# Optimization experiments

Measured on AMD Instinct MI355X. Metric: run time of the kernel, lower is better.

The kernel has to match this reference:

```python
import jax, jax.numpy as jnp
import numpy as np

F = 256      # n_features
N = 128      # n_nodes
B = 4096     # batch


def setup_inputs() -> dict:
    key = jax.random.key(0)
    ks = jax.random.split(key, 11)
    s = lambda *sh: 1.0 / np.sqrt(sh[-2]) if len(sh) >= 2 else 1.0
    x = jax.random.normal(ks[0], (B, F), dtype=jnp.float32)
    # Block-diagonal weights: [F, in, out] per stage; biases [F, out]
    w1 = jax.random.normal(ks[1], (F, 1, N), dtype=jnp.float32)
    b1 = jax.random.normal(ks[2], (F, N), dtype=jnp.float32) * 0.01
    w2 = jax.random.normal(ks[3], (F, N, N), dtype=jnp.float32) / np.sqrt(N)
    b2 = jax.random.normal(ks[4], (F, N), dtype=jnp.float32) * 0.01
    w3 = jax.random.normal(ks[5], (F, N, N), dtype=jnp.float32) / np.sqrt(N)
    b3 = jax.random.normal(ks[6], (F, N), dtype=jnp.float32) * 0.01
    w4 = jax.random.normal(ks[7], (F, N, 1), dtype=jnp.float32) / np.sqrt(N)
    b4 = jax.random.normal(ks[8], (F, 1), dtype=jnp.float32) * 0.01
    # Final linear: [F, 1] weight, [1] bias
    lr_w = jax.random.normal(ks[9], (F, 1), dtype=jnp.float32) / np.sqrt(F)
    lr_b = jax.random.normal(ks[10], (1,), dtype=jnp.float32) * 0.01
    return {"x": x, "w1": w1, "b1": b1, "w2": w2, "b2": b2,
            "w3": w3, "b3": b3, "w4": w4, "b4": b4,
            "lr_w": lr_w, "lr_b": lr_b}


def reference(x, w1, b1, w2, b2, w3, b3, w4, b4, lr_w, lr_b):
    # Per-feature block-diagonal MLP chain with ReLU between stages.
    # x: [B, F] -> view each feature as a 1-dim input to its own subnet.
    h = x[:, :, None]                                   # [B, F, 1]
    h = jax.nn.relu(jnp.einsum('bfi,fio->bfo', h, w1) + b1)   # [B, F, N]
    h = jax.nn.relu(jnp.einsum('bfi,fio->bfo', h, w2) + b2)   # [B, F, N]
    h = jax.nn.relu(jnp.einsum('bfi,fio->bfo', h, w3) + b3)   # [B, F, N]
    h = jnp.einsum('bfi,fio->bfo', h, w4) + b4                # [B, F, 1]
    x_pre = h[:, :, 0]                                        # [B, F]
    return x_pre @ lr_w + lr_b                                # [B, 1]
```

## Files before the change

### kernel.cpp

```cpp
#include <hip/hip_runtime.h>
#include <hip/hip_bf16.h>

#define F_DIM 256
#define N_DIM 128
#define B_DIM 4096

typedef float f32x2v __attribute__((ext_vector_type(2)));
typedef float f32x4v __attribute__((ext_vector_type(4)));
typedef float f32x16v __attribute__((ext_vector_type(16)));
typedef short s16x8 __attribute__((ext_vector_type(8)));
typedef unsigned int u32x4v __attribute__((ext_vector_type(4)));

#define PIN(x) asm("" : "+v"(x))

__device__ __forceinline__ unsigned short f2bf(float f) {
  union { float f; unsigned u; } v; v.f = f;
  unsigned r = v.u + 0x7fffu + ((v.u >> 16) & 1u);
  return (unsigned short)(r >> 16);
}

__device__ __forceinline__ unsigned pk2(float a, float b) {
  union { __hip_bfloat16 h[2]; unsigned u; } v;
  v.h[0] = __float2bfloat16(a);
  v.h[1] = __float2bfloat16(b);
  return v.u;
}

__device__ __forceinline__ void gload16(const void* g, void* l) {
  __builtin_amdgcn_global_load_lds(
      (const __attribute__((address_space(1))) unsigned int*)g,
      (__attribute__((address_space(3))) unsigned int*)l, 16, 0, 0);
}

__device__ __forceinline__ s16x8 frag1(unsigned d) {
  u32x4v v = {d, 0u, 0u, 0u};
  return __builtin_bit_cast(s16x8, v);
}

struct frag2 { s16x8 lo, hi; };

__device__ __forceinline__ frag2 cvt2(f32x16v a) {
  unsigned P[8];
#pragma unroll
  for (int q = 0; q < 8; ++q) {
    unsigned pk = pk2(a[2 * q], a[2 * q + 1]);
    asm("v_pk_max_i16 %0, %1, 0" : "=v"(P[q]) : "v"(pk));
  }
  u32x4v lo = {P[0], P[1], P[2], P[3]};
  u32x4v hh = {P[4], P[5], P[6], P[7]};
  frag2 r;
  r.lo = __builtin_bit_cast(s16x8, lo);
  r.hi = __builtin_bit_cast(s16x8, hh);
  return r;
}

__global__ void prep_w(const float* __restrict__ w2, const float* __restrict__ w3,
                       unsigned int* __restrict__ wTs) {
  __shared__ float tile[128 * 130];
  int m = blockIdx.x;
  const float* src = (m < 256) ? (w2 + (size_t)m * 16384)
                               : (w3 + (size_t)(m - 256) * 16384);
  int t = threadIdx.x;
  for (int k = 0; k < 64; ++k) {
    int idx = k * 256 + t;
    int i = idx >> 7, o = idx & 127;
    tile[o * 130 + i] = src[idx];
  }
  __syncthreads();
  unsigned int* dst = wTs + (size_t)m * 8192;
  for (int k = 0; k < 32; ++k) {
    int idx = k * 256 + t;
    int o = idx >> 6, i2 = idx & 63;
    unsigned pk = (unsigned)f2bf(tile[o * 130 + 2 * i2]) |
                  ((unsigned)f2bf(tile[o * 130 + 2 * i2 + 1]) << 16);
    int w = i2 & 7;
    int i2p = (i2 & ~7) + ((w >> 1) & 1) * 4 + (w & 1) + (((w >> 2) & 1) << 1);
    dst[(o * 64) + (i2p ^ ((o & 15) << 2))] = pk;
  }
}

__global__ void prep_x(const float* __restrict__ x, float* __restrict__ xT) {
  __shared__ float tile[64][65];
  int btile = blockIdx.x & 63;
  int ftile = blockIdx.x >> 6;
  int t = threadIdx.x;
  for (int k = 0; k < 16; ++k) {
    int idx = k * 256 + t;
    int r = idx >> 6, c = idx & 63;
    tile[r][c] = x[(size_t)(btile * 64 + r) * F_DIM + ftile * 64 + c];
  }
  __syncthreads();
  for (int k = 0; k < 16; ++k) {
    int idx = k * 256 + t;
    int fr = idx >> 6, br = idx & 63;
    xT[(size_t)(ftile * 64 + fr) * B_DIM + btile * 64 + br] = tile[br][fr];
  }
}

__global__ __launch_bounds__(512, 2) void mlp_chain(
    const float* __restrict__ xT, const float* __restrict__ w1,
    const float* __restrict__ b1, const float* __restrict__ b2,
    const float* __restrict__ b3, const float* __restrict__ w4,
    const float* __restrict__ b4, const unsigned int* __restrict__ wTs,
    float* __restrict__ xp) {
  __shared__ __align__(16) char Wb[2][128 * 256];
  __shared__ __align__(16) float w4l[N_DIM];

  const int f    = blockIdx.x >> 1;
  const int half = blockIdx.x & 1;
  const int t    = threadIdx.x;
  const int lane = t & 63, wid = t >> 6;
  const int c32 = lane & 31, hi = lane >> 5;

  {
    const char* s2 = (const char*)(wTs + (size_t)f * 8192);
    const char* s3 = (const char*)(wTs + (size_t)(256 + f) * 8192);
#pragma unroll
    for (int c = 0; c < 4; ++c) {
      int off = (wid * 4 + c) * 1024;
      gload16(s2 + off + lane * 16, &Wb[0][off]);
    }
#pragma unroll
    for (int c = 0; c < 4; ++c) {
      int off = (wid * 4 + c) * 1024;
      gload16(s3 + off + lane * 16, &Wb[1][off]);
    }
    if (t < 32) *(f32x4v*)&w4l[t * 4] = *(const f32x4v*)&w4[f * N_DIM + t * 4];
  }

  unsigned a1d[4], a2d[4], a3d[4];
#pragma unroll
  for (int it = 0; it < 4; ++it) {
    int i = it * 32 + c32;
    float w1v = w1[f * N_DIM + i], b1v = b1[f * N_DIM + i];
    float b2v = b2[f * N_DIM + i], b3v = b3[f * N_DIM + i];
    a1d[it] = hi ? 0u : pk2(w1v, b1v);
    a2d[it] = hi ? 0u : pk2(0.f, b2v);
    a3d[it] = hi ? 0u : pk2(0.f, b3v);
  }
  const float b4f = b4[f];
  const float* xcol = xT + (size_t)f * B_DIM + half * 2048;
  float* xprow = xp + (size_t)f * B_DIM + half * 2048;

  const int wbase = c32 * 256 + (((lane & 15) ^ hi) << 4);
  int va[8];
#pragma unroll
  for (int m = 0; m < 8; ++m) { va[m] = wbase ^ (m << 5); PIN(va[m]); }
  const char* wb = &Wb[0][0];

  __syncthreads();

  const f32x16v zero = {0.f, 0.f, 0.f, 0.f, 0.f, 0.f, 0.f, 0.f,
                        0.f, 0.f, 0.f, 0.f, 0.f, 0.f, 0.f, 0.f};
  const f32x2v zz = {0.f, 0.f};

  float xv = xcol[wid * 32 + c32];
#pragma unroll 1
  for (int itb = 0; itb < 8; ++itb) {
    const int bb = itb * 256 + wid * 32;
    s16x8 Bx = frag1(hi ? 0u : pk2(xv, 1.0f));
    float xv_n = (itb < 7) ? xcol[bb + 256 + c32] : 0.f;

    s16x8 h1[8];
#pragma unroll
    for (int it = 0; it < 4; ++it) {
      f32x16v h = __builtin_amdgcn_mfma_f32_32x32x16_bf16(frag1(a1d[it]), Bx,
                                                          zero, 0, 0, 0);
      frag2 r = cvt2(h);
      h1[2 * it] = r.lo;  h1[2 * it + 1] = r.hi;
      PIN(h1[2 * it]);  PIN(h1[2 * it + 1]);
    }

    s16x8 h2[8];
#pragma unroll
    for (int ntp = 0; ntp < 2; ++ntp) {
      const int nt0 = 2 * ntp, nt1 = nt0 + 1;
      f32x16v u0 = __builtin_amdgcn_mfma_f32_32x32x16_bf16(frag1(a2d[nt0]), Bx,
                                                           zero, 0, 0, 0);
      f32x16v u1 = __builtin_amdgcn_mfma_f32_32x32x16_bf16(frag1(a2d[nt1]), Bx,
                                                           zero, 0, 0, 0);
      __builtin_amdgcn_s_setprio(1);
#pragma unroll
      for (int m = 0; m < 8; ++m) {
        s16x8 af0 = *(const s16x8*)(wb + va[m] + nt0 * 8192);
        s16x8 af1 = *(const s16x8*)(wb + va[m] + nt1 * 8192);
        u0 = __builtin_amdgcn_mfma_f32_32x32x16_bf16(af0, h1[m], u0, 0, 0, 0);
        u1 = __builtin_amdgcn_mfma_f32_32x32x16_bf16(af1, h1[m], u1, 0, 0, 0);
      }
      __builtin_amdgcn_s_setprio(0);
      frag2 r0 = cvt2(u0);
      h2[2 * nt0] = r0.lo;  h2[2 * nt0 + 1] = r0.hi;
      PIN(h2[2 * nt0]);  PIN(h2[2 * nt0 + 1]);
      frag2 r1 = cvt2(u1);
      h2[2 * nt1] = r1.lo;  h2[2 * nt1 + 1] = r1.hi;
      PIN(h2[2 * nt1]);  PIN(h2[2 * nt1 + 1]);
    }

    f32x2v p0 = zz, p1 = zz;
#pragma unroll
    for (int n3p = 0; n3p < 2; ++n3p) {
      const int n30 = 2 * n3p, n31 = n30 + 1;
      f32x16v v0 = __builtin_amdgcn_mfma_f32_32x32x16_bf16(frag1(a3d[n30]), Bx,
                                                           zero, 0, 0, 0);
      f32x16v v1 = __builtin_amdgcn_mfma_f32_32x32x16_bf16(frag1(a3d[n31]), Bx,
                                                           zero, 0, 0, 0);
      __builtin_amdgcn_s_setprio(1);
#pragma unroll
      for (int k = 0; k < 8; ++k) {
        s16x8 af0 = *(const s16x8*)(wb + va[k] + 32768 + n30 * 8192);
        s16x8 af1 = *(const s16x8*)(wb + va[k] + 32768 + n31 * 8192);
        v0 = __builtin_amdgcn_mfma_f32_32x32x16_bf16(af0, h2[k], v0, 0, 0, 0);
        v1 = __builtin_amdgcn_mfma_f32_32x32x16_bf16(af1, h2[k], v1, 0, 0, 0);
      }
      __builtin_amdgcn_s_setprio(0);
#pragma unroll
      for (int q = 0; q < 4; ++q) {
        f32x2v w01_0 = *(const f32x2v*)&w4l[n30 * 32 + q * 8 + hi * 4];
        f32x2v w23_0 = *(const f32x2v*)&w4l[n30 * 32 + q * 8 + hi * 4 + 2];
        f32x2v w01_1 = *(const f32x2v*)&w4l[n31 * 32 + q * 8 + hi * 4];
        f32x2v w23_1 = *(const f32x2v*)&w4l[n31 * 32 + q * 8 + hi * 4 + 2];
        f32x2v r;
        r[0] = fmaxf(v0[4 * q + 0], 0.f); r[1] = fmaxf(v0[4 * q + 1], 0.f);
        p0 += r * w01_0;
        r[0] = fmaxf(v0[4 * q + 2], 0.f); r[1] = fmaxf(v0[4 * q + 3], 0.f);
        p1 += r * w23_0;
        r[0] = fmaxf(v1[4 * q + 0], 0.f); r[1] = fmaxf(v1[4 * q + 1], 0.f);
        p0 += r * w01_1;
        r[0] = fmaxf(v1[4 * q + 2], 0.f); r[1] = fmaxf(v1[4 * q + 3], 0.f);
        p1 += r * w23_1;
      }
    }
    float p = p0[0] + p0[1] + p1[0] + p1[1];
    p += __shfl_xor(p, 32, 64);
    if (hi == 0) xprow[bb + c32] = p + b4f;
    xv = xv_n;
  }
}

__global__ void final_reduce(const float* __restrict__ xp,
                             const float* __restrict__ lr_w,
                             const float* __restrict__ lr_b,
                             float* __restrict__ out) {
  __shared__ float lw[F_DIM];
  __shared__ float part[4][64];
  int t = threadIdx.x;
  if (t < F_DIM) lw[t] = lr_w[t];
  __syncthreads();
  int q = t >> 6, bl = t & 63;
  int b = blockIdx.x * 64 + bl;
  float acc = 0.f;
#pragma unroll 8
  for (int j = 0; j < 64; ++j) {
    int ff = q * 64 + j;
    acc += xp[(size_t)ff * B_DIM + b] * lw[ff];
  }
  part[q][bl] = acc;
  __syncthreads();
  if (q == 0)
    out[b] = part[0][bl] + part[1][bl] + part[2][bl] + part[3][bl] + lr_b[0];
}

extern "C" void kernel_launch(void* const* d_in, const int* in_sizes, int n_in,
                              void* d_out, int out_size, void* d_ws, size_t ws_size,
                              hipStream_t stream) {
  (void)in_sizes; (void)n_in; (void)out_size; (void)ws_size;
  const float* x    = (const float*)d_in[0];
  const float* w1   = (const float*)d_in[1];
  const float* b1   = (const float*)d_in[2];
  const float* w2   = (const float*)d_in[3];
  const float* b2   = (const float*)d_in[4];
  const float* w3   = (const float*)d_in[5];
  const float* b3   = (const float*)d_in[6];
  const float* w4   = (const float*)d_in[7];
  const float* b4   = (const float*)d_in[8];
  const float* lr_w = (const float*)d_in[9];
  const float* lr_b = (const float*)d_in[10];
  float* out = (float*)d_out;

  char* ws = (char*)d_ws;
  unsigned int* wTs = (unsigned int*)ws;
  float* xT = (float*)(ws + (16u << 20));
  float* xp = (float*)(ws + (16u << 20) + (4u << 20));

  prep_w<<<512, 256, 0, stream>>>(w2, w3, wTs);
  prep_x<<<256, 256, 0, stream>>>(x, xT);
  mlp_chain<<<512, 512, 0, stream>>>(xT, w1, b1, b2, b3, w4, b4, wTs, xp);
  final_reduce<<<64, 256, 0, stream>>>(xp, lr_w, lr_b, out);
}
```

Baseline: 99.25 us.

## Keep per-feature W2/W3 fragments in registers and split output columns across waves

Restructures the MLP kernel so that each of 4 waves owns one 32-column output tile of W2 and W3 and holds those weight fragments in registers, instead of staging the full weights in LDS and reading them on every batch tile. The layer-2 output is exchanged through a small LDS buffer with a block barrier, and the layer-4 partial sums are reduced across waves through shared memory. The grid grows to 8 blocks per feature, each covering 512 batch rows. This removes repeated LDS weight reads, but adds two __syncthreads per batch tile, reloads W2/W3 from global memory in every block, and drops the prefetch of x.

```diff
diff --git a/kernel.cpp b/kernel.cpp
--- a/kernel.cpp
+++ b/kernel.cpp
@@ -24,12 +24,6 @@
   v.h[0] = __float2bfloat16(a);
   v.h[1] = __float2bfloat16(b);
   return v.u;
-}
-
-__device__ __forceinline__ void gload16(const void* g, void* l) {
-  __builtin_amdgcn_global_load_lds(
-      (const __attribute__((address_space(1))) unsigned int*)g,
-      (__attribute__((address_space(3))) unsigned int*)l, 16, 0, 0);
 }
 
 __device__ __forceinline__ s16x8 frag1(unsigned d) {
@@ -97,56 +91,47 @@
   }
 }
 
-__global__ __launch_bounds__(512, 2) void mlp_chain(
+__global__ __launch_bounds__(256, 3) void mlp_wreg(
     const float* __restrict__ xT, const float* __restrict__ w1,
     const float* __restrict__ b1, const float* __restrict__ b2,
     const float* __restrict__ b3, const float* __restrict__ w4,
     const float* __restrict__ b4, const unsigned int* __restrict__ wTs,
     float* __restrict__ xp) {
-  __shared__ __align__(16) char Wb[2][128 * 256];
+  __shared__ __align__(16) char xch[8192];
   __shared__ __align__(16) float w4l[N_DIM];
-
-  const int f    = blockIdx.x >> 1;
-  const int half = blockIdx.x & 1;
-  const int t    = threadIdx.x;
+  __shared__ float part[4][32];
+
+  const int f  = blockIdx.x >> 3;
+  const int oc = blockIdx.x & 7;
+  const int t  = threadIdx.x;
   const int lane = t & 63, wid = t >> 6;
   const int c32 = lane & 31, hi = lane >> 5;
 
-  {
-    const char* s2 = (const char*)(wTs + (size_t)f * 8192);
-    const char* s3 = (const char*)(wTs + (size_t)(256 + f) * 8192);
-#pragma unroll
-    for (int c = 0; c < 4; ++c) {
-      int off = (wid * 4 + c) * 1024;
-      gload16(s2 + off + lane * 16, &Wb[0][off]);
-    }
-#pragma unroll
-    for (int c = 0; c < 4; ++c) {
-      int off = (wid * 4 + c) * 1024;
-      gload16(s3 + off + lane * 16, &Wb[1][off]);
-    }
-    if (t < 32) *(f32x4v*)&w4l[t * 4] = *(const f32x4v*)&w4[f * N_DIM + t * 4];
-  }
-
-  unsigned a1d[4], a2d[4], a3d[4];
+  if (t < 32) *(f32x4v*)&w4l[t * 4] = *(const f32x4v*)&w4[f * N_DIM + t * 4];
+
+  const int wbase = c32 * 256 + (((lane & 15) ^ hi) << 4);
+  const char* wsrc2 = (const char*)wTs + (size_t)f * 32768 + wid * 8192;
+  const char* wsrc3 = (const char*)wTs + (size_t)(256 + f) * 32768 + wid * 8192;
+  s16x8 w2f[8], w3f[8];
+#pragma unroll
+  for (int m = 0; m < 8; ++m) {
+    int a = wbase ^ (m << 5);
+    w2f[m] = *(const s16x8*)(wsrc2 + a);  PIN(w2f[m]);
+    w3f[m] = *(const s16x8*)(wsrc3 + a);  PIN(w3f[m]);
+  }
+
+  unsigned a1d[4];
 #pragma unroll
   for (int it = 0; it < 4; ++it) {
     int i = it * 32 + c32;
-    float w1v = w1[f * N_DIM + i], b1v = b1[f * N_DIM + i];
-    float b2v = b2[f * N_DIM + i], b3v = b3[f * N_DIM + i];
-    a1d[it] = hi ? 0u : pk2(w1v, b1v);
-    a2d[it] = hi ? 0u : pk2(0.f, b2v);
-    a3d[it] = hi ? 0u : pk2(0.f, b3v);
-  }
+    a1d[it] = hi ? 0u : pk2(w1[f * N_DIM + i], b1[f * N_DIM + i]);
+  }
+  const unsigned a2d = hi ? 0u : pk2(0.f, b2[f * N_DIM + wid * 32 + c32]);
+  const unsigned a3d = hi ? 0u : pk2(0.f, b3[f * N_DIM + wid * 32 + c32]);
   const float b4f = b4[f];
-  const float* xcol = xT + (size_t)f * B_DIM + half * 2048;
-  float* xprow = xp + (size_t)f * B_DIM + half * 2048;
-
-  const int wbase = c32 * 256 + (((lane & 15) ^ hi) << 4);
-  int va[8];
-#pragma unroll
-  for (int m = 0; m < 8; ++m) { va[m] = wbase ^ (m << 5); PIN(va[m]); }
-  const char* wb = &Wb[0][0];
+
+  const float* xcol = xT + (size_t)f * B_DIM + oc * 512;
+  float* xprow = xp + (size_t)f * B_DIM + oc * 512;
 
   __syncthreads();
 
@@ -154,12 +139,11 @@
                         0.f, 0.f, 0.f, 0.f, 0.f, 0.f, 0.f, 0.f};
   const f32x2v zz = {0.f, 0.f};
 
-  float xv = xcol[wid * 32 + c32];
 #pragma unroll 1
-  for (int itb = 0; itb < 8; ++itb) {
-    const int bb = itb * 256 + wid * 32;
+  for (int itb = 0; itb < 16; ++itb) {
+    const int bb = itb * 32;
+    float xv = xcol[bb + c32];
     s16x8 Bx = frag1(hi ? 0u : pk2(xv, 1.0f));
-    float xv_n = (itb < 7) ? xcol[bb + 256 + c32] : 0.f;
 
     s16x8 h1[8];
 #pragma unroll
@@ -171,69 +155,49 @@
       PIN(h1[2 * it]);  PIN(h1[2 * it + 1]);
     }
 
+    f32x16v u = __builtin_amdgcn_mfma_f32_32x32x16_bf16(frag1(a2d), Bx,
+                                                        zero, 0, 0, 0);
+    __builtin_amdgcn_s_setprio(1);
+#pragma unroll
+    for (int m = 0; m < 8; ++m)
+      u = __builtin_amdgcn_mfma_f32_32x32x16_bf16(w2f[m], h1[m], u, 0, 0, 0);
+    __builtin_amdgcn_s_setprio(0);
+    frag2 r2 = cvt2(u);
+
+    *(s16x8*)(xch + (wid * 2 + 0) * 1024 + lane * 16) = r2.lo;
+    *(s16x8*)(xch + (wid * 2 + 1) * 1024 + lane * 16) = r2.hi;
+    __syncthreads();
+
     s16x8 h2[8];
 #pragma unroll
-    for (int ntp = 0; ntp < 2; ++ntp) {
-      const int nt0 = 2 * ntp, nt1 = nt0 + 1;
-      f32x16v u0 = __builtin_amdgcn_mfma_f32_32x32x16_bf16(frag1(a2d[nt0]), Bx,
-                                                           zero, 0, 0, 0);
-      f32x16v u1 = __builtin_amdgcn_mfma_f32_32x32x16_bf16(frag1(a2d[nt1]), Bx,
-                                                           zero, 0, 0, 0);
-      __builtin_amdgcn_s_setprio(1);
-#pragma unroll
-      for (int m = 0; m < 8; ++m) {
-        s16x8 af0 = *(const s16x8*)(wb + va[m] + nt0 * 8192);
-        s16x8 af1 = *(const s16x8*)(wb + va[m] + nt1 * 8192);
-        u0 = __builtin_amdgcn_mfma_f32_32x32x16_bf16(af0, h1[m], u0, 0, 0, 0);
-        u1 = __builtin_amdgcn_mfma_f32_32x32x16_bf16(af1, h1[m], u1, 0, 0, 0);
-      }
-      __builtin_amdgcn_s_setprio(0);
-      frag2 r0 = cvt2(u0);
-      h2[2 * nt0] = r0.lo;  h2[2 * nt0 + 1] = r0.hi;
-      PIN(h2[2 * nt0]);  PIN(h2[2 * nt0 + 1]);
-      frag2 r1 = cvt2(u1);
-      h2[2 * nt1] = r1.lo;  h2[2 * nt1 + 1] = r1.hi;
-      PIN(h2[2 * nt1]);  PIN(h2[2 * nt1 + 1]);
-    }
+    for (int k = 0; k < 8; ++k)
+      h2[k] = *(const s16x8*)(xch + k * 1024 + lane * 16);
+
+    f32x16v v = __builtin_amdgcn_mfma_f32_32x32x16_bf16(frag1(a3d), Bx,
+                                                        zero, 0, 0, 0);
+    __builtin_amdgcn_s_setprio(1);
+#pragma unroll
+    for (int k = 0; k < 8; ++k)
+      v = __builtin_amdgcn_mfma_f32_32x32x16_bf16(w3f[k], h2[k], v, 0, 0, 0);
+    __builtin_amdgcn_s_setprio(0);
 
     f32x2v p0 = zz, p1 = zz;
 #pragma unroll
-    for (int n3p = 0; n3p < 2; ++n3p) {
-      const int n30 = 2 * n3p, n31 = n30 + 1;
-      f32x16v v0 = __builtin_amdgcn_mfma_f32_32x32x16_bf16(frag1(a3d[n30]), Bx,
-                                                           zero, 0, 0, 0);
-      f32x16v v1 = __builtin_amdgcn_mfma_f32_32x32x16_bf16(frag1(a3d[n31]), Bx,
-                                                           zero, 0, 0, 0);
-      __builtin_amdgcn_s_setprio(1);
-#pragma unroll
-      for (int k = 0; k < 8; ++k) {
-        s16x8 af0 = *(const s16x8*)(wb + va[k] + 32768 + n30 * 8192);
-        s16x8 af1 = *(const s16x8*)(wb + va[k] + 32768 + n31 * 8192);
-        v0 = __builtin_amdgcn_mfma_f32_32x32x16_bf16(af0, h2[k], v0, 0, 0, 0);
-        v1 = __builtin_amdgcn_mfma_f32_32x32x16_bf16(af1, h2[k], v1, 0, 0, 0);
-      }
-      __builtin_amdgcn_s_setprio(0);
-#pragma unroll
-      for (int q = 0; q < 4; ++q) {
-        f32x2v w01_0 = *(const f32x2v*)&w4l[n30 * 32 + q * 8 + hi * 4];
-        f32x2v w23_0 = *(const f32x2v*)&w4l[n30 * 32 + q * 8 + hi * 4 + 2];
-        f32x2v w01_1 = *(const f32x2v*)&w4l[n31 * 32 + q * 8 + hi * 4];
-        f32x2v w23_1 = *(const f32x2v*)&w4l[n31 * 32 + q * 8 + hi * 4 + 2];
-        f32x2v r;
-        r[0] = fmaxf(v0[4 * q + 0], 0.f); r[1] = fmaxf(v0[4 * q + 1], 0.f);
-        p0 += r * w01_0;
-        r[0] = fmaxf(v0[4 * q + 2], 0.f); r[1] = fmaxf(v0[4 * q + 3], 0.f);
-        p1 += r * w23_0;
-        r[0] = fmaxf(v1[4 * q + 0], 0.f); r[1] = fmaxf(v1[4 * q + 1], 0.f);
-        p0 += r * w01_1;
-        r[0] = fmaxf(v1[4 * q + 2], 0.f); r[1] = fmaxf(v1[4 * q + 3], 0.f);
-        p1 += r * w23_1;
-      }
+    for (int q = 0; q < 4; ++q) {
+      f32x2v w01 = *(const f32x2v*)&w4l[wid * 32 + q * 8 + hi * 4];
+      f32x2v w23 = *(const f32x2v*)&w4l[wid * 32 + q * 8 + hi * 4 + 2];
+      f32x2v r;
+      r[0] = fmaxf(v[4 * q + 0], 0.f); r[1] = fmaxf(v[4 * q + 1], 0.f);
+      p0 += r * w01;
+      r[0] = fmaxf(v[4 * q + 2], 0.f); r[1] = fmaxf(v[4 * q + 3], 0.f);
+      p1 += r * w23;
     }
     float p = p0[0] + p0[1] + p1[0] + p1[1];
     p += __shfl_xor(p, 32, 64);
-    if (hi == 0) xprow[bb + c32] = p + b4f;
-    xv = xv_n;
+    if (hi == 0) part[wid][c32] = p;
+    __syncthreads();
+    if (t < 32)
+      xprow[bb + t] = part[0][t] + part[1][t] + part[2][t] + part[3][t] + b4f;
   }
 }
 
@@ -284,6 +248,6 @@
 
   prep_w<<<512, 256, 0, stream>>>(w2, w3, wTs);
   prep_x<<<256, 256, 0, stream>>>(x, xT);
-  mlp_chain<<<512, 512, 0, stream>>>(xT, w1, b1, b2, b3, w4, b4, wTs, xp);
+  mlp_wreg<<<2048, 256, 0, stream>>>(xT, w1, b1, b2, b3, w4, b4, wTs, xp);
   final_reduce<<<64, 256, 0, stream>>>(xp, lr_w, lr_b, out);
 }
```

After: 133.8 us. +34.8%, slower.
